# Optimization experiments

Measured on AMD Instinct MI355X. Metric: run time of the kernel, lower is better.

Reference implementation:

```python
import jax, jax.numpy as jnp
import numpy as np

IN_SIZE = 512
HID = 512
BATCH = 65536


def setup_inputs() -> dict:
    key = jax.random.key(0)
    ks = jax.random.split(key, 20)
    s = 1.0 / np.sqrt(IN_SIZE)
    sh = 1.0 / np.sqrt(HID)
    d = {
        "inputs": jax.random.normal(ks[0], (BATCH, IN_SIZE), jnp.float32),
        "state": jax.random.normal(ks[1], (BATCH, HID), jnp.float32),
        "parent_state": jax.random.normal(ks[2], (BATCH, HID), jnp.float32),
    }
    # input-path linears (with bias), torch Linear layout: W [out, in], y = x @ W.T + b
    for i, name in enumerate(["w_a", "w_r", "w_r1", "w_c"]):
        d[name + "_w"] = jax.random.uniform(ks[3 + 2 * i], (HID, IN_SIZE), jnp.float32, -s, s)
        d[name + "_b"] = jax.random.uniform(ks[4 + 2 * i], (HID,), jnp.float32, -s, s)
    # state-path and parent-path linears (no bias)
    for i, name in enumerate(["u_a", "u_r", "u_r1", "u_c", "p_a", "p_r", "p_r1", "p_c"]):
        d[name + "_w"] = jax.random.uniform(ks[11 + i], (HID, HID), jnp.float32, -sh, sh)
    return d


def reference(inputs, state, parent_state,
              w_a_w, w_a_b, w_r_w, w_r_b, w_r1_w, w_r1_b, w_c_w, w_c_b,
              u_a_w, u_r_w, u_r1_w, u_c_w,
              p_a_w, p_r_w, p_r1_w, p_c_w):
    def lin(x, w, b=None):
        y = x @ w.T
        return y if b is None else y + b

    att = jax.nn.sigmoid(lin(inputs, w_a_w, w_a_b) + lin(state, u_a_w) + lin(parent_state, p_a_w))
    r = jax.nn.sigmoid(lin(inputs, w_r_w, w_r_b) + lin(state, u_r_w) + lin(parent_state, p_r_w))
    r1 = jax.nn.sigmoid(lin(inputs, w_r1_w, w_r1_b) + lin(state, u_r1_w) + lin(parent_state, p_r1_w))
    c = jnp.tanh(lin(inputs, w_c_w, w_c_b) + lin(state * r, u_c_w) + lin(parent_state * r1, p_c_w))
    new_h = att * c + (1.0 - att) * state
    return new_h
```

## Files before the change

kernel.cpp:

```cpp
#include <hip/hip_runtime.h>
#include <stdint.h>


typedef unsigned short u16;
using bf16x8 = __attribute__((ext_vector_type(8))) __bf16;
using f32x4  = __attribute__((ext_vector_type(4))) float;

__device__ __forceinline__ u16 f2bf(float f) {
    __bf16 b = (__bf16)f;
    union { __bf16 b; u16 u; } v; v.b = b;
    return v.u;
}
__device__ __forceinline__ uint32_t f2bf2(float lo, float hi) {
    return (uint32_t)f2bf(lo) | ((uint32_t)f2bf(hi) << 16);
}
__device__ __forceinline__ float bf2f(u16 s) {
    union { uint32_t u; float f; } v; v.u = ((uint32_t)s) << 16;
    return v.f;
}
__device__ __forceinline__ void load_lds16(const void* g, void* l) {
    __builtin_amdgcn_global_load_lds(
        (const __attribute__((address_space(1))) uint32_t*)g,
        (__attribute__((address_space(3))) uint32_t*)l, 16, 0, 0);
}
__device__ __forceinline__ void fence_bar() {
    asm volatile("" ::: "memory");
    __builtin_amdgcn_s_barrier();
    asm volatile("" ::: "memory");
}

__global__ void prep_weights(
    const float* __restrict__ wa, const float* __restrict__ ua, const float* __restrict__ pa,
    const float* __restrict__ wrg, const float* __restrict__ ur, const float* __restrict__ pr,
    const float* __restrict__ wr1, const float* __restrict__ ur1, const float* __restrict__ pr1,
    const float* __restrict__ wcc, const float* __restrict__ uc, const float* __restrict__ pc,
    u16* __restrict__ B1, u16* __restrict__ B2)
{
    int idx = blockIdx.x * 256 + threadIdx.x;
    const int T1 = 1536 * 1536;
    if (idx < T1) {
        int n = idx / 1536, k = idx - n * 1536;
        int g = n >> 9, nn = n & 511;
        int o = k >> 9, kk = k & 511;
        const float* s;
        if (g == 0)      s = (o == 0) ? wa  : (o == 1) ? ua  : pa;
        else if (g == 1) s = (o == 0) ? wrg : (o == 1) ? ur  : pr;
        else             s = (o == 0) ? wr1 : (o == 1) ? ur1 : pr1;
        B1[idx] = f2bf(s[nn * 512 + kk]);
    } else {
        int j = idx - T1;
        if (j < 512 * 1536) {
            int n = j / 1536, k = j - n * 1536;
            int o = k >> 9, kk = k & 511;
            const float* s = (o == 0) ? wcc : (o == 1) ? uc : pc;
            B2[j] = f2bf(s[n * 512 + kk]);
        }
    }
}

__global__ void cast_inputs(const float* __restrict__ X, const float* __restrict__ H,
                            const float* __restrict__ P,
                            u16* __restrict__ Xb, u16* __restrict__ Hb, u16* __restrict__ Pb)
{
    const long long MAT8 = (65536LL * 512) / 8;
    for (long long t = (long long)blockIdx.x * 256 + threadIdx.x;
         t < 3 * MAT8; t += (long long)gridDim.x * 256) {
        int m = (int)(t >> 22);
        long long e = (t & (MAT8 - 1)) * 8;
        const float* s = (m == 0) ? X : (m == 1) ? H : P;
        u16* d = (m == 0) ? Xb : (m == 1) ? Hb : Pb;
        f32x4 a = *(const f32x4*)(s + e);
        f32x4 b = *(const f32x4*)(s + e + 4);
        uint4 q;
        q.x = f2bf2(a.x, a.y); q.y = f2bf2(a.z, a.w);
        q.z = f2bf2(b.x, b.y); q.w = f2bf2(b.z, b.w);
        *(uint4*)(d + e) = q;
    }
}

template<int MODE>
__global__ __launch_bounds__(512, 2)
void gemm256(const u16* __restrict__ A0, const u16* __restrict__ A1s, const u16* __restrict__ A2s,
             const u16* __restrict__ Bw,
             const float* __restrict__ bias0, const float* __restrict__ bias1,
             const float* __restrict__ bias2,
             const u16* __restrict__ HbP, const u16* __restrict__ PbP,
             const float* __restrict__ Hf,
             float* __restrict__ outp, u16* __restrict__ hrw, u16* __restrict__ pr1w)
{
    __shared__ u16 lds[65536];
    constexpr int NT = 24;

    const int tid  = threadIdx.x;
    const int lane = tid & 63;
    const int wv   = tid >> 6;
    const int wr   = wv >> 2;
    const int wc   = wv & 3;

    int panel, ntl;
    const int xcd = blockIdx.x & 7;
    const int idx = blockIdx.x >> 3;
    if (MODE == 1) { panel = xcd * 32 + idx / 6;    ntl = idx % 6; }
    else           { panel = xcd * 32 + (idx >> 1); ntl = idx & 1; }
    const int m0 = panel * 256;
    const int n0 = ntl * 256;

    const int srow = tid >> 3;
    const int scg  = ((tid & 7) ^ (srow & 7)) * 8;
    const int ldst = srow * 64 + (tid & 7) * 8;

    const int ofsA = srow * 512 + scg;
    const int ofsB = srow * 1536 + scg;
    const u16* const bA0 = A0  + (size_t)m0 * 512;
    const u16* const bA1 = A1s + (size_t)m0 * 512;
    const u16* const bA2 = A2s + (size_t)m0 * 512;
    const u16* const bB  = Bw  + (size_t)n0 * 1536;
    u16* const ldA = lds + ldst;
    u16* const ldB = lds + 16384 + ldst;

    const int fr = lane & 15;
    const int fk = (lane >> 4) * 8;
    const int sw = (lane & 7) * 8;
    const int c0 = fk ^ sw;
    const int c1 = (32 + fk) ^ sw;
    const int aOff = (wr * 128 + fr) * 64;
    const int bOff = 16384 + (wc * 64 + fr) * 64;

    f32x4 acc[8][4];
    const f32x4 vzero = {0.0f, 0.0f, 0.0f, 0.0f};
#pragma unroll
    for (int i = 0; i < 8; ++i)
#pragma unroll
        for (int j = 0; j < 4; ++j) acc[i][j] = vzero;

    auto stA = [&](int T) {
        const u16* src = (T < 8) ? bA0 : (T < 16) ? bA1 : bA2;
        const u16* g = src + (T & 7) * 64 + ofsA;
        u16* l = ldA + (T & 1) * 32768;
        load_lds16(g,             l);
        load_lds16(g +  64 * 512, l + 4096);
        load_lds16(g + 128 * 512, l + 8192);
        load_lds16(g + 192 * 512, l + 12288);
    };
    auto stB = [&](int T) {
        const u16* g = bB + T * 64 + ofsB;
        u16* l = ldB + (T & 1) * 32768;
        load_lds16(g,              l);
        load_lds16(g +  64 * 1536, l + 4096);
        load_lds16(g + 128 * 1536, l + 8192);
        load_lds16(g + 192 * 1536, l + 12288);
    };

    stA(0); stB(0);
    stA(1); stB(1);
    asm volatile("s_waitcnt vmcnt(8)" ::: "memory");
    fence_bar();

    for (int T = 0; T < NT; ++T) {
        const int cb = (T & 1) * 32768;
        const u16* const pa0 = lds + (cb + aOff + c0);
        const u16* const pa1 = lds + (cb + aOff + c1);
        const u16* const pb0 = lds + (cb + bOff + c0);
        const u16* const pb1 = lds + (cb + bOff + c1);

        bf16x8 bF[4][2];
#pragma unroll
        for (int j = 0; j < 4; ++j) {
            bF[j][0] = *(const bf16x8*)(pb0 + j * 1024);
            bF[j][1] = *(const bf16x8*)(pb1 + j * 1024);
        }
        bf16x8 aF0[4][2];
#pragma unroll
        for (int m = 0; m < 4; ++m) {
            aF0[m][0] = *(const bf16x8*)(pa0 + m * 1024);
            aF0[m][1] = *(const bf16x8*)(pa1 + m * 1024);
        }
        __builtin_amdgcn_s_setprio(1);
#pragma unroll
        for (int m = 0; m < 4; ++m)
#pragma unroll
            for (int j = 0; j < 4; ++j)
#pragma unroll
                for (int ks = 0; ks < 2; ++ks)
                    acc[m][j] = __builtin_amdgcn_mfma_f32_16x16x32_bf16(
                        aF0[m][ks], bF[j][ks], acc[m][j], 0, 0, 0);
        __builtin_amdgcn_s_setprio(0);
        bf16x8 aF1[4][2];
#pragma unroll
        for (int m = 0; m < 4; ++m) {
            aF1[m][0] = *(const bf16x8*)(pa0 + (4 + m) * 1024);
            aF1[m][1] = *(const bf16x8*)(pa1 + (4 + m) * 1024);
        }
        __builtin_amdgcn_s_setprio(1);
#pragma unroll
        for (int m = 0; m < 4; ++m)
#pragma unroll
            for (int j = 0; j < 4; ++j)
#pragma unroll
                for (int ks = 0; ks < 2; ++ks)
                    acc[4 + m][j] = __builtin_amdgcn_mfma_f32_16x16x32_bf16(
                        aF1[m][ks], bF[j][ks], acc[4 + m][j], 0, 0, 0);
        __builtin_amdgcn_s_setprio(0);

        fence_bar();
        if (T < NT - 2) {
            stA(T + 2); stB(T + 2);
            asm volatile("s_waitcnt vmcnt(8)" ::: "memory");
        } else if (T == NT - 2) {
            asm volatile("s_waitcnt vmcnt(0)" ::: "memory");
        }
        fence_bar();
    }

    const int rbase = m0 + wr * 128 + (lane >> 4) * 4;
    if (MODE == 1) {
        const int g = ntl >> 1;
        const float* bias = (g == 0) ? bias0 : (g == 1) ? bias1 : bias2;
        const int ncb = (ntl & 1) * 256 + wc * 64;
#pragma unroll
        for (int i = 0; i < 8; ++i)
#pragma unroll
            for (int j = 0; j < 4; ++j) {
                const int nn = ncb + j * 16 + fr;
                const float b = bias[nn];
                int off = (rbase + i * 16) * 512 + nn;
#pragma unroll
                for (int jj = 0; jj < 4; ++jj, off += 512) {
                    float v = acc[i][j][jj] + b;
                    float s = 1.0f / (1.0f + __expf(-v));
                    if (g == 0)      outp[off] = s;
                    else if (g == 1) hrw[off]  = f2bf(s * bf2f(HbP[off]));
                    else             pr1w[off] = f2bf(s * bf2f(PbP[off]));
                }
            }
    } else {
        const int ncb = n0 + wc * 64;
#pragma unroll
        for (int i = 0; i < 8; ++i)
#pragma unroll
            for (int j = 0; j < 4; ++j) {
                const int nn = ncb + j * 16 + fr;
                const float b = bias0[nn];
                int off = (rbase + i * 16) * 512 + nn;
#pragma unroll
                for (int jj = 0; jj < 4; ++jj, off += 512) {
                    float v = acc[i][j][jj] + b;
                    float e = __expf(2.0f * v);
                    float ct = 1.0f - 2.0f / (e + 1.0f);
                    float a = outp[off];
                    outp[off] = a * ct + (1.0f - a) * Hf[off];
                }
            }
    }
}

__global__ __launch_bounds__(256, 2)
void k1_small(const float* __restrict__ X, const float* __restrict__ H,
              const float* __restrict__ P, const u16* __restrict__ B1,
              const float* __restrict__ ba, const float* __restrict__ br,
              const float* __restrict__ br1,
              float* __restrict__ attf, u16* __restrict__ hrw, u16* __restrict__ pr1w)
{
    __shared__ u16 Ab[2][128 * 64];
    __shared__ u16 Bb[2][128 * 64];
    const int tid = threadIdx.x, lane = tid & 63, w = tid >> 6;
    const int wr = w >> 1, wc = w & 1;
    const int bid = blockIdx.x, xcd = bid & 7, idx = bid >> 3;
    const int panel = idx / 12, ntl = idx - panel * 12;
    const int m0 = (xcd * 64 + panel) * 128, n0 = ntl * 128;
    const int srow = w * 32 + (lane >> 3);
    const int scol = ((lane & 7) ^ (lane >> 3)) * 8;
    const int arow = tid >> 4, acol = (tid & 15) * 4;
    const int aswz = acol ^ ((arow & 7) << 3);
    f32x4 acc[4][4];
    const f32x4 vz = {0, 0, 0, 0};
#pragma unroll
    for (int i = 0; i < 4; ++i)
#pragma unroll
        for (int j = 0; j < 4; ++j) acc[i][j] = vz;
    f32x4 areg[8];
    auto issueA = [&](int kt) {
        const float* src = (kt < 8) ? X : (kt < 16) ? H : P;
        const float* base = src + (size_t)(m0 + arow) * 512 + (kt & 7) * 64 + acol;
#pragma unroll
        for (int rr = 0; rr < 8; ++rr)
            areg[rr] = *(const f32x4*)(base + (size_t)(rr * 16) * 512);
    };
    auto writeA = [&](int nb) {
#pragma unroll
        for (int rr = 0; rr < 8; ++rr) {
            uint2 q; q.x = f2bf2(areg[rr].x, areg[rr].y);
            q.y = f2bf2(areg[rr].z, areg[rr].w);
            *(uint2*)&Ab[nb][(arow + rr * 16) * 64 + aswz] = q;
        }
    };
    auto issueB = [&](int kt, int nb) {
        const u16* gb = B1 + (size_t)(n0 + srow) * 1536 + kt * 64 + scol;
        u16* lb = &Bb[nb][(w * 32) * 64];
#pragma unroll
        for (int c = 0; c < 4; ++c)
            load_lds16(gb + (size_t)c * 8 * 1536, lb + c * 8 * 64);
    };
    auto compute = [&](int cb) {
        const int rsw = (lane & 7) << 3, rb = lane & 15, hi8 = (lane >> 4) * 8;
#pragma unroll
        for (int ks = 0; ks < 2; ++ks) {
            bf16x8 af[4], bfr[4];
            const int col = (ks * 32 + hi8) ^ rsw;
#pragma unroll
            for (int fm = 0; fm < 4; ++fm)
                af[fm] = *(const bf16x8*)&Ab[cb][(wr * 64 + fm * 16 + rb) * 64 + col];
#pragma unroll
            for (int fn = 0; fn < 4; ++fn)
                bfr[fn] = *(const bf16x8*)&Bb[cb][(wc * 64 + fn * 16 + rb) * 64 + col];
#pragma unroll
            for (int fm = 0; fm < 4; ++fm)
#pragma unroll
                for (int fn = 0; fn < 4; ++fn)
                    acc[fm][fn] = __builtin_amdgcn_mfma_f32_16x16x32_bf16(
                        af[fm], bfr[fn], acc[fm][fn], 0, 0, 0);
        }
    };
    issueA(0); issueB(0, 0); writeA(0);
    __syncthreads();
    int cb = 0;
#pragma unroll 2
    for (int kt = 0; kt < 24; ++kt) {
        if (kt < 23) { issueA(kt + 1); issueB(kt + 1, cb ^ 1); }
        compute(cb);
        if (kt < 23) writeA(cb ^ 1);
        __syncthreads();
        cb ^= 1;
    }
    const int gate = ntl >> 2;
    const float* bias = (gate == 0) ? ba : (gate == 1) ? br : br1;
    const int nnb = (ntl & 3) * 128 + wc * 64;
    const int rl = (lane >> 4) * 4, cl = lane & 15;
#pragma unroll
    for (int fm = 0; fm < 4; ++fm)
#pragma unroll
        for (int fn = 0; fn < 4; ++fn) {
            const int nn = nnb + fn * 16 + cl;
            const float b = bias[nn];
#pragma unroll
            for (int j = 0; j < 4; ++j) {
                const int row = m0 + wr * 64 + fm * 16 + rl + j;
                const size_t off = (size_t)row * 512 + nn;
                float v = acc[fm][fn][j] + b;
                float s = 1.0f / (1.0f + __expf(-v));
                if (gate == 0)      attf[off] = s;
                else if (gate == 1) hrw[off]  = f2bf(s * H[off]);
                else                pr1w[off] = f2bf(s * P[off]);
            }
        }
}

__global__ __launch_bounds__(256, 2)
void k2_small(const float* __restrict__ X, const float* __restrict__ H,
              const u16* __restrict__ B2, const float* __restrict__ bc,
              const u16* __restrict__ hrw, const u16* __restrict__ pr1w,
              float* outp)
{
    __shared__ u16 Ab[2][128 * 64];
    __shared__ u16 Bb[2][128 * 64];
    const int tid = threadIdx.x, lane = tid & 63, w = tid >> 6;
    const int wr = w >> 1, wc = w & 1;
    const int bid = blockIdx.x, xcd = bid & 7, idx = bid >> 3;
    const int panel = idx >> 2, ntl = idx & 3;
    const int m0 = (xcd * 64 + panel) * 128, n0 = ntl * 128;
    const int srow = w * 32 + (lane >> 3);
    const int scol = ((lane & 7) ^ (lane >> 3)) * 8;
    const int arow = tid >> 4, acol = (tid & 15) * 4;
    const int aswz = acol ^ ((arow & 7) << 3);
    f32x4 acc[4][4];
    const f32x4 vz = {0, 0, 0, 0};
#pragma unroll
    for (int i = 0; i < 4; ++i)
#pragma unroll
        for (int j = 0; j < 4; ++j) acc[i][j] = vz;
    f32x4 areg[8];
    auto issueA = [&](int kt, int nb) {
        if (kt >= 8) {
            const u16* src = (kt < 16) ? hrw : pr1w;
            const u16* gb = src + (size_t)(m0 + srow) * 512 + (kt & 7) * 64 + scol;
            u16* lb = &Ab[nb][(w * 32) * 64];
#pragma unroll
            for (int c = 0; c < 4; ++c)
                load_lds16(gb + (size_t)c * 8 * 512, lb + c * 8 * 64);
        } else {
            const float* base = X + (size_t)(m0 + arow) * 512 + (kt & 7) * 64 + acol;
#pragma unroll
            for (int rr = 0; rr < 8; ++rr)
                areg[rr] = *(const f32x4*)(base + (size_t)(rr * 16) * 512);
        }
    };
    auto writeA = [&](int kt, int nb) {
        if (kt < 8) {
#pragma unroll
            for (int rr = 0; rr < 8; ++rr) {
                uint2 q; q.x = f2bf2(areg[rr].x, areg[rr].y);
                q.y = f2bf2(areg[rr].z, areg[rr].w);
                *(uint2*)&Ab[nb][(arow + rr * 16) * 64 + aswz] = q;
            }
        }
    };
    auto issueB = [&](int kt, int nb) {
        const u16* gb = B2 + (size_t)(n0 + srow) * 1536 + kt * 64 + scol;
        u16* lb = &Bb[nb][(w * 32) * 64];
#pragma unroll
        for (int c = 0; c < 4; ++c)
            load_lds16(gb + (size_t)c * 8 * 1536, lb + c * 8 * 64);
    };
    auto compute = [&](int cb) {
        const int rsw = (lane & 7) << 3, rb = lane & 15, hi8 = (lane >> 4) * 8;
#pragma unroll
        for (int ks = 0; ks < 2; ++ks) {
            bf16x8 af[4], bfr[4];
            const int col = (ks * 32 + hi8) ^ rsw;
#pragma unroll
            for (int fm = 0; fm < 4; ++fm)
                af[fm] = *(const bf16x8*)&Ab[cb][(wr * 64 + fm * 16 + rb) * 64 + col];
#pragma unroll
            for (int fn = 0; fn < 4; ++fn)
                bfr[fn] = *(const bf16x8*)&Bb[cb][(wc * 64 + fn * 16 + rb) * 64 + col];
#pragma unroll
            for (int fm = 0; fm < 4; ++fm)
#pragma unroll
                for (int fn = 0; fn < 4; ++fn)
                    acc[fm][fn] = __builtin_amdgcn_mfma_f32_16x16x32_bf16(
                        af[fm], bfr[fn], acc[fm][fn], 0, 0, 0);
        }
    };
    issueA(0, 0); issueB(0, 0); writeA(0, 0);
    __syncthreads();
    int cb = 0;
#pragma unroll 2
    for (int kt = 0; kt < 24; ++kt) {
        if (kt < 23) { issueA(kt + 1, cb ^ 1); issueB(kt + 1, cb ^ 1); }
        compute(cb);
        if (kt < 23) writeA(kt + 1, cb ^ 1);
        __syncthreads();
        cb ^= 1;
    }
    const int nnb = n0 + wc * 64;
    const int rl = (lane >> 4) * 4, cl = lane & 15;
#pragma unroll
    for (int fm = 0; fm < 4; ++fm)
#pragma unroll
        for (int fn = 0; fn < 4; ++fn) {
            const int nn = nnb + fn * 16 + cl;
            const float b = bc[nn];
#pragma unroll
            for (int j = 0; j < 4; ++j) {
                const int row = m0 + wr * 64 + fm * 16 + rl + j;
                const size_t off = (size_t)row * 512 + nn;
                float v = acc[fm][fn][j] + b;
                float e = __expf(2.0f * v);
                float ct = 1.0f - 2.0f / (e + 1.0f);
                float a = outp[off];
                outp[off] = a * ct + (1.0f - a) * H[off];
            }
        }
}

extern "C" void kernel_launch(void* const* d_in, const int* in_sizes, int n_in,
                              void* d_out, int out_size, void* d_ws, size_t ws_size,
                              hipStream_t stream)
{
    const float* X   = (const float*)d_in[0];
    const float* H   = (const float*)d_in[1];
    const float* P   = (const float*)d_in[2];
    const float* wa  = (const float*)d_in[3];
    const float* ba  = (const float*)d_in[4];
    const float* wrg = (const float*)d_in[5];
    const float* br  = (const float*)d_in[6];
    const float* wr1 = (const float*)d_in[7];
    const float* br1 = (const float*)d_in[8];
    const float* wcc = (const float*)d_in[9];
    const float* bc  = (const float*)d_in[10];
    const float* ua  = (const float*)d_in[11];
    const float* ur  = (const float*)d_in[12];
    const float* ur1 = (const float*)d_in[13];
    const float* uc  = (const float*)d_in[14];
    const float* pa  = (const float*)d_in[15];
    const float* pr  = (const float*)d_in[16];
    const float* pr1 = (const float*)d_in[17];
    const float* pc  = (const float*)d_in[18];

    char* ws = (char*)d_ws;
    u16* B1   = (u16*)(ws);
    u16* B2   = (u16*)(ws + (size_t)4718592);
    u16* hrp  = (u16*)(ws + (size_t)6291456);
    u16* pr1p = (u16*)(ws + (size_t)73400320);
    u16* Xb   = (u16*)(ws + (size_t)140509184);
    u16* Hb   = (u16*)(ws + (size_t)207618048);
    u16* Pb   = (u16*)(ws + (size_t)274726912);
    float* out = (float*)d_out;

    const bool big = ws_size >= (size_t)341835776ULL;

    prep_weights<<<12288, 256, 0, stream>>>(wa, ua, pa, wrg, ur, pr, wr1, ur1, pr1,
                                            wcc, uc, pc, B1, B2);
    if (big) {
        cast_inputs<<<3072, 256, 0, stream>>>(X, H, P, Xb, Hb, Pb);
        gemm256<1><<<1536, 512, 0, stream>>>(Xb, Hb, Pb, B1, ba, br, br1,
                                             Hb, Pb, nullptr, out, hrp, pr1p);
        gemm256<2><<<512, 512, 0, stream>>>(Xb, hrp, pr1p, B2, bc, nullptr, nullptr,
                                            nullptr, nullptr, H, out, nullptr, nullptr);
    } else {
        k1_small<<<6144, 256, 0, stream>>>(X, H, P, B1, ba, br, br1, out, hrp, pr1p);
        k2_small<<<2048, 256, 0, stream>>>(X, H, B2, bc, hrp, pr1p, out);
    }
}
```

Baseline: 799.0 us.

## Split GEMM K-loop into half-phases with staggered A/B prefetch, read bf16 state

Restructures the gemm256 main loop into two half-phases per K-tile. The A tile for the next step and the B tile two steps ahead are issued between the phases, with explicit lgkmcnt waits and sched_barriers around the MFMA blocks, and the loop is no longer unrolled. The aim is to spread global-to-LDS traffic across the iteration and overlap it better with MFMA work. Separately, the final blend now reads the state from the bf16 copy instead of the fp32 tensor, halving that epilogue read but lowering the precision of the (1-att)*state term. The extra barriers per iteration could add synchronisation cost, and single-buffered A reuse could create a race if the barrier placement is wrong.

```diff
diff --git a/kernel.cpp b/kernel.cpp
--- a/kernel.cpp
+++ b/kernel.cpp
@@ -85,7 +85,6 @@
              const float* __restrict__ bias0, const float* __restrict__ bias1,
              const float* __restrict__ bias2,
              const u16* __restrict__ HbP, const u16* __restrict__ PbP,
-             const float* __restrict__ Hf,
              float* __restrict__ outp, u16* __restrict__ hrw, u16* __restrict__ pr1w)
 {
     __shared__ u16 lds[65536];
@@ -152,10 +151,11 @@
     };
 
     stA(0); stB(0);
-    stA(1); stB(1);
-    asm volatile("s_waitcnt vmcnt(8)" ::: "memory");
+    stB(1);
+    asm volatile("s_waitcnt vmcnt(4)" ::: "memory");
     fence_bar();
 
+#pragma unroll 1
     for (int T = 0; T < NT; ++T) {
         const int cb = (T & 1) * 32768;
         const u16* const pa0 = lds + (cb + aOff + c0);
@@ -169,47 +169,55 @@
             bF[j][0] = *(const bf16x8*)(pb0 + j * 1024);
             bF[j][1] = *(const bf16x8*)(pb1 + j * 1024);
         }
-        bf16x8 aF0[4][2];
-#pragma unroll
-        for (int m = 0; m < 4; ++m) {
-            aF0[m][0] = *(const bf16x8*)(pa0 + m * 1024);
-            aF0[m][1] = *(const bf16x8*)(pa1 + m * 1024);
-        }
-        __builtin_amdgcn_s_setprio(1);
-#pragma unroll
-        for (int m = 0; m < 4; ++m)
-#pragma unroll
-            for (int j = 0; j < 4; ++j)
-#pragma unroll
-                for (int ks = 0; ks < 2; ++ks)
-                    acc[m][j] = __builtin_amdgcn_mfma_f32_16x16x32_bf16(
-                        aF0[m][ks], bF[j][ks], acc[m][j], 0, 0, 0);
-        __builtin_amdgcn_s_setprio(0);
-        bf16x8 aF1[4][2];
-#pragma unroll
-        for (int m = 0; m < 4; ++m) {
-            aF1[m][0] = *(const bf16x8*)(pa0 + (4 + m) * 1024);
-            aF1[m][1] = *(const bf16x8*)(pa1 + (4 + m) * 1024);
-        }
-        __builtin_amdgcn_s_setprio(1);
-#pragma unroll
-        for (int m = 0; m < 4; ++m)
-#pragma unroll
-            for (int j = 0; j < 4; ++j)
-#pragma unroll
-                for (int ks = 0; ks < 2; ++ks)
-                    acc[4 + m][j] = __builtin_amdgcn_mfma_f32_16x16x32_bf16(
-                        aF1[m][ks], bF[j][ks], acc[4 + m][j], 0, 0, 0);
-        __builtin_amdgcn_s_setprio(0);
-
-        fence_bar();
-        if (T < NT - 2) {
-            stA(T + 2); stB(T + 2);
-            asm volatile("s_waitcnt vmcnt(8)" ::: "memory");
-        } else if (T == NT - 2) {
-            asm volatile("s_waitcnt vmcnt(0)" ::: "memory");
-        }
-        fence_bar();
+        {
+            bf16x8 aF[4][2];
+#pragma unroll
+            for (int m = 0; m < 4; ++m) {
+                aF[m][0] = *(const bf16x8*)(pa0 + m * 1024);
+                aF[m][1] = *(const bf16x8*)(pa1 + m * 1024);
+            }
+            if (T < NT - 1) stA(T + 1);
+            fence_bar();
+            asm volatile("s_waitcnt lgkmcnt(0)" ::: "memory");
+            __builtin_amdgcn_sched_barrier(0);
+            __builtin_amdgcn_s_setprio(1);
+#pragma unroll
+            for (int m = 0; m < 4; ++m)
+#pragma unroll
+                for (int j = 0; j < 4; ++j)
+#pragma unroll
+                    for (int ks = 0; ks < 2; ++ks)
+                        acc[m][j] = __builtin_amdgcn_mfma_f32_16x16x32_bf16(
+                            aF[m][ks], bF[j][ks], acc[m][j], 0, 0, 0);
+            __builtin_amdgcn_s_setprio(0);
+            fence_bar();
+        }
+
+        {
+            bf16x8 aG[4][2];
+#pragma unroll
+            for (int m = 0; m < 4; ++m) {
+                aG[m][0] = *(const bf16x8*)(pa0 + (4 + m) * 1024);
+                aG[m][1] = *(const bf16x8*)(pa1 + (4 + m) * 1024);
+            }
+            if (T < NT - 2) stB(T + 2);
+            fence_bar();
+            asm volatile("s_waitcnt lgkmcnt(0)" ::: "memory");
+            __builtin_amdgcn_sched_barrier(0);
+            __builtin_amdgcn_s_setprio(1);
+#pragma unroll
+            for (int m = 0; m < 4; ++m)
+#pragma unroll
+                for (int j = 0; j < 4; ++j)
+#pragma unroll
+                    for (int ks = 0; ks < 2; ++ks)
+                        acc[4 + m][j] = __builtin_amdgcn_mfma_f32_16x16x32_bf16(
+                            aG[m][ks], bF[j][ks], acc[4 + m][j], 0, 0, 0);
+            __builtin_amdgcn_s_setprio(0);
+            if (T < NT - 2)       asm volatile("s_waitcnt vmcnt(4)" ::: "memory");
+            else if (T == NT - 2) asm volatile("s_waitcnt vmcnt(0)" ::: "memory");
+            fence_bar();
+        }
     }
 
     const int rbase = m0 + wr * 128 + (lane >> 4) * 4;
@@ -248,7 +256,8 @@
                     float e = __expf(2.0f * v);
                     float ct = 1.0f - 2.0f / (e + 1.0f);
                     float a = outp[off];
-                    outp[off] = a * ct + (1.0f - a) * Hf[off];
+                    float h = bf2f(HbP[off]);
+                    outp[off] = a * ct + (1.0f - a) * h;
                 }
             }
     }
@@ -504,9 +513,9 @@
     if (big) {
         cast_inputs<<<3072, 256, 0, stream>>>(X, H, P, Xb, Hb, Pb);
         gemm256<1><<<1536, 512, 0, stream>>>(Xb, Hb, Pb, B1, ba, br, br1,
-                                             Hb, Pb, nullptr, out, hrp, pr1p);
+                                             Hb, Pb, out, hrp, pr1p);
         gemm256<2><<<512, 512, 0, stream>>>(Xb, hrp, pr1p, B2, bc, nullptr, nullptr,
-                                            nullptr, nullptr, H, out, nullptr, nullptr);
+                                            Hb, nullptr, out, nullptr, nullptr);
     } else {
         k1_small<<<6144, 256, 0, stream>>>(X, H, P, B1, ba, br, br1, out, hrp, pr1p);
         k2_small<<<2048, 256, 0, stream>>>(X, H, B2, bc, hrp, pr1p, out);
```

After: 738.6 us. -7.6%, faster.
